# Optimization experiments

Hardware: AMD Instinct MI355X
Metric: run time of the kernel (lower is better)

The kernel has to match this reference:

```python
import jax, jax.numpy as jnp
import numpy as np


def _three_nn(parent_xyz, xyz):
    # parent_xyz: (bs, n, 3) queries; xyz: (bs, m, 3) reference points.
    # Squared pairwise distances (bs, n, m) without forming (x-y)^2 tensor of rank 4.
    d2 = (jnp.sum(parent_xyz**2, -1, keepdims=True)
          - 2.0 * jnp.einsum('bnd,bmd->bnm', parent_xyz, xyz)
          + jnp.sum(xyz**2, -1)[:, None, :])
    neg_d2, idx = jax.lax.top_k(-d2, 3)           # 3 smallest distances
    dist = jnp.sqrt(jnp.maximum(-neg_d2, 0.0))    # pointnet2 returns sqrt(dist2)
    return dist, idx                              # (bs, n, 3), (bs, n, 3)


def _three_interpolate(feats, idx, weight):
    # feats: (bs, c, m); idx, weight: (bs, n, 3) -> (bs, c, n)
    feats_t = jnp.swapaxes(feats, 1, 2)                     # (bs, m, c)
    gathered = jax.vmap(lambda f, i: f[i])(feats_t, idx)    # (bs, n, 3, c)
    out = jnp.einsum('bnkc,bnk->bcn', gathered, weight)
    return out


def _conv1x1(x, W, b):
    # x: (bs, c_in, n); W: (c_out, c_in); b: (c_out,)
    return jnp.einsum('oc,bcn->bon', W, x) + b[None, :, None]


def setup_inputs() -> dict:
    key = jax.random.key(0)
    ks = jax.random.split(key, 6)
    bs, m, n = 8, 1024, 4096
    c0, c1, c2 = 256, 128, 256
    xyz = jax.random.normal(ks[0], (bs, m, 3), jnp.float32)
    parent_xyz = jax.random.normal(ks[1], (bs, n, 3), jnp.float32)
    feats = jax.random.normal(ks[2], (bs, c0, m), jnp.float32)
    skip_feats = jax.random.normal(ks[3], (bs, c1, n), jnp.float32)
    W1 = jax.random.normal(ks[4], (c2, c0 + c1), jnp.float32) * (1.0 / np.sqrt(c0 + c1))
    b1 = jnp.zeros((c2,), jnp.float32)
    W2 = jax.random.normal(ks[5], (c2, c2), jnp.float32) * (1.0 / np.sqrt(c2))
    b2 = jnp.zeros((c2,), jnp.float32)
    return {"xyz": xyz, "parent_xyz": parent_xyz, "feats": feats,
            "skip_feats": skip_feats, "W1": W1, "b1": b1, "W2": W2, "b2": b2}


def reference(xyz, parent_xyz, feats, skip_feats, W1, b1, W2, b2):
    dist, idx = _three_nn(parent_xyz, xyz)
    inv_dist = 1.0 / (dist + 1e-8)
    weight = inv_dist / jnp.sum(inv_dist, 2, keepdims=True)     # (bs, n, 3)
    up_feats = _three_interpolate(feats, idx, weight)           # (bs, c0, n)
    parent_feats = jnp.concatenate([up_feats, skip_feats], 1)   # (bs, c0+c1, n)
    h = jax.nn.relu(_conv1x1(parent_feats, W1, b1))
    out = jax.nn.relu(_conv1x1(h, W2, b2))
    return out
```

## Files before the change

kernel.cpp:

```cpp
#include <hip/hip_runtime.h>
#include <hip/hip_bf16.h>
#include <cstddef>
#include <cstdint>

#define BS    8
#define M_PTS 1024
#define N_PTS 4096
#define C0    256
#define C1    128
#define C2    256
#define K1DIM 384

typedef __attribute__((ext_vector_type(8))) short bf16x8;
typedef __attribute__((ext_vector_type(4))) float f32x4;
typedef __attribute__((ext_vector_type(2))) float f32x2;

__device__ __forceinline__ ushort f2bf(float f) {
  union { float f; unsigned u; } v; v.f = f;
  unsigned r = v.u + 0x7fffu + ((v.u >> 16) & 1u);
  return (ushort)(r >> 16);
}

__device__ __forceinline__ float rdlane_f(float v, int lane) {
  union { float f; int i; } u; u.f = v;
  u.i = __builtin_amdgcn_readlane(u.i, lane);
  return u.f;
}

__device__ __forceinline__ f32x2 pk_mul(f32x2 a, f32x2 b) {
  f32x2 r; asm("v_pk_mul_f32 %0, %1, %2" : "=v"(r) : "v"(a), "v"(b)); return r;
}
__device__ __forceinline__ f32x2 pk_add(f32x2 a, f32x2 b) {
  f32x2 r; asm("v_pk_add_f32 %0, %1, %2" : "=v"(r) : "v"(a), "v"(b)); return r;
}

__global__ __launch_bounds__(256) void prep_k(
    const float* __restrict__ feats, const float* __restrict__ W1,
    const float* __restrict__ W2, float* __restrict__ featsT,
    ushort* __restrict__ W1f, ushort* __restrict__ W2f) {
  __shared__ float tile[32][33];
  const int t = threadIdx.x;
  if (blockIdx.x < 2048) {
    const int bx = blockIdx.x & 31;
    const int by = (blockIdx.x >> 5) & 7;
    const int bz = blockIdx.x >> 8;
    const int tx = t & 31, ty = t >> 5;
    const float* ip = feats + (size_t)bz * C0 * M_PTS;
    float*       op = featsT + (size_t)bz * C0 * M_PTS;
    const int r0 = by * 32, c0 = bx * 32;
#pragma unroll
    for (int i = 0; i < 4; ++i)
      tile[ty + i * 8][tx] = ip[(size_t)(r0 + ty + i * 8) * M_PTS + c0 + tx];
    __syncthreads();
#pragma unroll
    for (int i = 0; i < 4; ++i)
      op[(size_t)(c0 + ty + i * 8) * C0 + r0 + tx] = tile[tx][ty + i * 8];
  } else {
    const int id = (blockIdx.x - 2048) * 256 + t;
    if (id < C2 * K1DIM) {
      int m = id / K1DIM, k = id - m * K1DIM;
      int off = (((m >> 4) * 12 + (k >> 5)) * 4 + ((k >> 3) & 3)) * 128 + (m & 15) * 8 + (k & 7);
      W1f[off] = f2bf(W1[id]);
    }
    if (id < C2 * C2) {
      int m = id >> 8, k = id & 255;
      int off = (((m >> 4) * 8 + (k >> 5)) * 4 + ((k >> 3) & 3)) * 128 + (m & 15) * 8 + (k & 7);
      W2f[off] = f2bf(W2[id]);
    }
  }
}

__global__ __launch_bounds__(256, 4) void fp_fused_k(
    const float* __restrict__ xyz,
    const float* __restrict__ pxyz,
    const float* __restrict__ featsT,
    const float* __restrict__ skip,
    const ushort* __restrict__ W1f,
    const float* __restrict__ b1,
    const ushort* __restrict__ W2f,
    const float* __restrict__ b2,
    float* __restrict__ out) {
  __shared__ float4 smemq[2560];
  float4* pts4 = smemq;
  ushort* pfB  = (ushort*)(smemq + 1024);
  ushort* hbuf = (ushort*)smemq;

  const int t  = threadIdx.x;
  const int b  = blockIdx.x & 7;
  const int n0 = (blockIdx.x >> 3) * 32;
  const int wv = t >> 6, l = t & 63;
  const int q  = t >> 3, sub = t & 7;

  const float qx = pxyz[((size_t)b * N_PTS + n0 + q) * 3 + 0];
  const float qy = pxyz[((size_t)b * N_PTS + n0 + q) * 3 + 1];
  const float qz = pxyz[((size_t)b * N_PTS + n0 + q) * 3 + 2];

#pragma unroll
  for (int it = 0; it < 2; ++it) {
    const int p = t + it * 256;
    const float2* xb = (const float2*)(xyz + (size_t)b * 3 * M_PTS + 6 * p);
    const float2 A = xb[0], B = xb[1], C = xb[2];
    const float x0 = A.x, y0 = A.y, z0 = B.x, x1 = B.y, y1 = C.x, z1 = C.y;
    const float s0 = __fadd_rn(__fadd_rn(__fmul_rn(x0, x0), __fmul_rn(y0, y0)),
                               __fmul_rn(z0, z0));
    const float s1 = __fadd_rn(__fadd_rn(__fmul_rn(x1, x1), __fmul_rn(y1, y1)),
                               __fmul_rn(z1, z1));
    const int U = p ^ ((p >> 6) & 7);
    pts4[U * 2 + 0] = (float4){x0, x1, y0, y1};
    pts4[U * 2 + 1] = (float4){z0, z1, s0, s1};
  }

  float skp[16];
#pragma unroll
  for (int it = 0; it < 8; ++it) {
    const int id = t + it * 256;
    const int r2 = id >> 5, nn = id & 31;
    skp[2 * it + 0] = skip[((size_t)b * C1 + 2 * r2 + 0) * N_PTS + n0 + nn];
    skp[2 * it + 1] = skip[((size_t)b * C1 + 2 * r2 + 1) * N_PTS + n0 + nn];
  }

  const float qq = __fadd_rn(__fadd_rn(__fmul_rn(qx, qx), __fmul_rn(qy, qy)),
                             __fmul_rn(qz, qz));
  __syncthreads();

  float d0 = 3.4e38f, d1 = 3.4e38f, d2 = 3.4e38f;
  int   i0 = 0, i1 = 0, i2 = 0;
  {
    const f32x2 Qx2 = {qx, qx}, Qy2 = {qy, qy}, Qz2 = {qz, qz};
    const f32x2 Qq2 = {qq, qq}, Mn2 = {-2.0f, -2.0f};
    int pe[8];
#pragma unroll
    for (int e = 0; e < 8; ++e) pe[e] = (sub * 64 + (e ^ sub)) * 2;
    for (int jb = 0; jb < 8; ++jb) {
#pragma unroll
      for (int e = 0; e < 8; ++e) {
        const float4 lo = pts4[pe[e] + jb * 16];
        const float4 hi = pts4[pe[e] + jb * 16 + 1];
        const f32x2 Xp = {lo.x, lo.y}, Yp = {lo.z, lo.w};
        const f32x2 Zp = {hi.x, hi.y}, Sp = {hi.z, hi.w};
        const f32x2 dotp = pk_add(pk_add(pk_mul(Qx2, Xp), pk_mul(Qy2, Yp)),
                                  pk_mul(Qz2, Zp));
        const f32x2 dp = pk_add(pk_add(Qq2, pk_mul(dotp, Mn2)), Sp);
        {
          const float d = dp.x; const int m = jb * 16 + 2 * e;
          const bool c0 = d < d0, c1 = d < d1, c2 = d < d2;
          i2 = c1 ? i1 : (c2 ? m : i2);
          i1 = c0 ? i0 : (c1 ? m : i1);
          i0 = c0 ? m : i0;
          d2 = __builtin_amdgcn_fmed3f(d, d1, d2);
          d1 = __builtin_amdgcn_fmed3f(d, d0, d1);
          d0 = fminf(d, d0);
        }
        {
          const float d = dp.y; const int m = jb * 16 + 2 * e + 1;
          const bool c0 = d < d0, c1 = d < d1, c2 = d < d2;
          i2 = c1 ? i1 : (c2 ? m : i2);
          i1 = c0 ? i0 : (c1 ? m : i1);
          i0 = c0 ? m : i0;
          d2 = __builtin_amdgcn_fmed3f(d, d1, d2);
          d1 = __builtin_amdgcn_fmed3f(d, d0, d1);
          d0 = fminf(d, d0);
        }
      }
    }
    i0 += sub * 128; i1 += sub * 128; i2 += sub * 128;
  }

#pragma unroll
  for (int mk = 1; mk <= 4; mk <<= 1) {
    const float pd0 = __shfl_xor(d0, mk), pd1 = __shfl_xor(d1, mk), pd2 = __shfl_xor(d2, mk);
    const int   pi0 = __shfl_xor(i0, mk), pi1 = __shfl_xor(i1, mk), pi2 = __shfl_xor(i2, mk);
    const bool lo = (sub & mk) == 0;
    const float a0 = lo ? d0 : pd0, a1 = lo ? d1 : pd1, a2 = lo ? d2 : pd2;
    const float b0 = lo ? pd0 : d0, b1v = lo ? pd1 : d1, b2v = lo ? pd2 : d2;
    const int   A0 = lo ? i0 : pi0, A1 = lo ? i1 : pi1, A2 = lo ? i2 : pi2;
    const int   B0 = lo ? pi0 : i0, B1 = lo ? pi1 : i1, B2 = lo ? pi2 : i2;
    const bool c0 = b0 < a0;
    const bool cb1a0 = b1v < a0, cb0a1 = b0 < a1;
    const bool cb1a1 = b1v < a1, cb2a0 = b2v < a0, cb0a2 = b0 < a2;
    const float m0 = c0 ? b0 : a0;                 const int M0 = c0 ? B0 : A0;
    const float t1a = cb1a0 ? b1v : a0;            const int T1a = cb1a0 ? B1 : A0;
    const float t1b = cb0a1 ? b0 : a1;             const int T1b = cb0a1 ? B0 : A1;
    const float m1 = c0 ? t1a : t1b;               const int M1 = c0 ? T1a : T1b;
    const float sA = cb2a0 ? b2v : a0;             const int SA = cb2a0 ? B2 : A0;
    const float sB = cb1a1 ? b1v : a1;             const int SB = cb1a1 ? B1 : A1;
    const float sD = cb0a2 ? b0 : a2;              const int SD = cb0a2 ? B0 : A2;
    const float m2 = c0 ? (cb1a0 ? sA : sB) : (cb0a1 ? sB : sD);
    const int   M2 = c0 ? (cb1a0 ? SA : SB) : (cb0a1 ? SB : SD);
    d0 = m0; d1 = m1; d2 = m2; i0 = M0; i1 = M1; i2 = M2;
  }

  float w0f, w1f, w2f;
  {
    const float t0 = sqrtf(fmaxf(d0, 0.f)), t1 = sqrtf(fmaxf(d1, 0.f)),
                t2 = sqrtf(fmaxf(d2, 0.f));
    const float r0 = 1.0f / (t0 + 1e-8f), r1 = 1.0f / (t1 + 1e-8f),
                r2 = 1.0f / (t2 + 1e-8f);
    const float rs = __fadd_rn(__fadd_rn(r0, r1), r2);
    w0f = r0 / rs; w1f = r1 / rs; w2f = r2 / rs;
  }

  {
    const float* fb = featsT + (size_t)b * M_PTS * C0;
#pragma unroll
    for (int qi = 0; qi < 8; ++qi) {
      const int src = qi * 8;
      const int  j0 = __builtin_amdgcn_readlane(i0, src);
      const int  j1 = __builtin_amdgcn_readlane(i1, src);
      const int  j2 = __builtin_amdgcn_readlane(i2, src);
      const float w0 = rdlane_f(w0f, src), w1 = rdlane_f(w1f, src), w2 = rdlane_f(w2f, src);
      const float4 f0 = *(const float4*)(fb + (size_t)j0 * C0 + l * 4);
      const float4 f1 = *(const float4*)(fb + (size_t)j1 * C0 + l * 4);
      const float4 f2 = *(const float4*)(fb + (size_t)j2 * C0 + l * 4);
      ushort4 hv;
      hv.x = f2bf(w0 * f0.x + w1 * f1.x + w2 * f2.x);
      hv.y = f2bf(w0 * f0.y + w1 * f1.y + w2 * f2.y);
      hv.z = f2bf(w0 * f0.z + w1 * f1.z + w2 * f2.z);
      hv.w = f2bf(w0 * f0.w + w1 * f1.w + w2 * f2.w);
      const int nq = wv * 8 + qi;
      const int kq = l >> 1;
      const int u = kq * 32 + (nq ^ (kq & 7));
      *reinterpret_cast<ushort4*>(&pfB[u * 8 + (l & 1) * 4]) = hv;
    }
  }
#pragma unroll
  for (int it = 0; it < 8; ++it) {
    const int id = t + it * 256;
    const int r2 = id >> 5, nn = id & 31;
    const int k = C0 + 2 * r2;
    const int kq = k >> 3;
    const int u = kq * 32 + (nn ^ (kq & 7));
    ushort2 sv; sv.x = f2bf(skp[2 * it]); sv.y = f2bf(skp[2 * it + 1]);
    *reinterpret_cast<ushort2*>(&pfB[u * 8 + (k & 7)]) = sv;
  }
  __syncthreads();

  const int c = l & 15, g = l >> 4;

  f32x4 acc[4][2];
#pragma unroll
  for (int i = 0; i < 4; ++i)
#pragma unroll
    for (int j = 0; j < 2; ++j) acc[i][j] = (f32x4){0.f, 0.f, 0.f, 0.f};

  for (int kb = 0; kb < 12; ++kb) {
    const int kqg = kb * 4 + g;
    bf16x8 bfr[2], afr[4];
#pragma unroll
    for (int j = 0; j < 2; ++j)
      bfr[j] = *reinterpret_cast<const bf16x8*>(&pfB[(kqg * 32 + ((j * 16 + c) ^ (kqg & 7))) * 8]);
#pragma unroll
    for (int i = 0; i < 4; ++i)
      afr[i] = *reinterpret_cast<const bf16x8*>(&W1f[(((wv * 4 + i) * 12 + kb) * 4 + g) * 128 + c * 8]);
    __builtin_amdgcn_s_setprio(1);
#pragma unroll
    for (int i = 0; i < 4; ++i)
#pragma unroll
      for (int j = 0; j < 2; ++j)
        acc[i][j] = __builtin_amdgcn_mfma_f32_16x16x32_bf16(afr[i], bfr[j], acc[i][j], 0, 0, 0);
    __builtin_amdgcn_s_setprio(0);
  }

#pragma unroll
  for (int i = 0; i < 4; ++i) {
    const int mbase = wv * 64 + i * 16 + g * 4;
    const float4 bias = *(const float4*)(b1 + mbase);
#pragma unroll
    for (int j = 0; j < 2; ++j) {
      const int nn = j * 16 + c;
      const int kq = mbase >> 3;
      const int u = kq * 32 + (nn ^ (kq & 7));
      ushort4 hv;
      hv.x = f2bf(fmaxf(acc[i][j].x + bias.x, 0.f));
      hv.y = f2bf(fmaxf(acc[i][j].y + bias.y, 0.f));
      hv.z = f2bf(fmaxf(acc[i][j].z + bias.z, 0.f));
      hv.w = f2bf(fmaxf(acc[i][j].w + bias.w, 0.f));
      *reinterpret_cast<ushort4*>(&hbuf[u * 8 + (mbase & 7)]) = hv;
    }
  }
  __syncthreads();

#pragma unroll
  for (int i = 0; i < 4; ++i)
#pragma unroll
    for (int j = 0; j < 2; ++j) acc[i][j] = (f32x4){0.f, 0.f, 0.f, 0.f};

  for (int kb = 0; kb < 8; ++kb) {
    const int kqg = kb * 4 + g;
    bf16x8 bfr[2], afr[4];
#pragma unroll
    for (int j = 0; j < 2; ++j)
      bfr[j] = *reinterpret_cast<const bf16x8*>(&hbuf[(kqg * 32 + ((j * 16 + c) ^ (kqg & 7))) * 8]);
#pragma unroll
    for (int i = 0; i < 4; ++i)
      afr[i] = *reinterpret_cast<const bf16x8*>(&W2f[(((wv * 4 + i) * 8 + kb) * 4 + g) * 128 + c * 8]);
    __builtin_amdgcn_s_setprio(1);
#pragma unroll
    for (int i = 0; i < 4; ++i)
#pragma unroll
      for (int j = 0; j < 2; ++j)
        acc[i][j] = __builtin_amdgcn_mfma_f32_16x16x32_bf16(afr[i], bfr[j], acc[i][j], 0, 0, 0);
    __builtin_amdgcn_s_setprio(0);
  }

#pragma unroll
  for (int i = 0; i < 4; ++i) {
    const int mbase = wv * 64 + i * 16 + g * 4;
    const float4 bias = *(const float4*)(b2 + mbase);
#pragma unroll
    for (int j = 0; j < 2; ++j) {
      const int nn = n0 + j * 16 + c;
      out[((size_t)b * C2 + mbase + 0) * N_PTS + nn] = fmaxf(acc[i][j].x + bias.x, 0.f);
      out[((size_t)b * C2 + mbase + 1) * N_PTS + nn] = fmaxf(acc[i][j].y + bias.y, 0.f);
      out[((size_t)b * C2 + mbase + 2) * N_PTS + nn] = fmaxf(acc[i][j].z + bias.z, 0.f);
      out[((size_t)b * C2 + mbase + 3) * N_PTS + nn] = fmaxf(acc[i][j].w + bias.w, 0.f);
    }
  }
}

extern "C" void kernel_launch(void* const* d_in, const int* in_sizes, int n_in,
                              void* d_out, int out_size, void* d_ws, size_t ws_size,
                              hipStream_t stream) {
  const float* xyz   = (const float*)d_in[0];
  const float* pxyz  = (const float*)d_in[1];
  const float* feats = (const float*)d_in[2];
  const float* skip  = (const float*)d_in[3];
  const float* W1    = (const float*)d_in[4];
  const float* b1    = (const float*)d_in[5];
  const float* W2    = (const float*)d_in[6];
  const float* b2    = (const float*)d_in[7];
  float* out = (float*)d_out;

  float*  ws     = (float*)d_ws;
  float*  featsT = ws;
  ushort* W1f    = (ushort*)(featsT + (size_t)BS * M_PTS * C0);
  ushort* W2f    = W1f + (size_t)C2 * K1DIM;

  prep_k<<<2432, 256, 0, stream>>>(feats, W1, W2, featsT, W1f, W2f);
  fp_fused_k<<<BS * (N_PTS / 32), 256, 0, stream>>>(xyz, pxyz, featsT, skip,
                                                    W1f, b1, W2f, b2, out);
}
```

Measured before the change: 47.06 us.

## Split fused kernel into separate three-NN scan and GEMM kernels

Splits the single fused kernel into a nearest-neighbor scan kernel (16 queries per block, 16 lanes per query, occupancy hint of 8) and a GEMM kernel that reads indices and weights from a workspace buffer. The aim is to cut the register and LDS pressure of the fused kernel so each phase can run at higher occupancy. In exchange it adds a kernel launch and a round trip of indices and weights through global memory. It also adds a barrier before the hbuf writes, and skip loads are no longer held in registers across the scan.

```diff
diff --git a/kernel.cpp b/kernel.cpp
--- a/kernel.cpp
+++ b/kernel.cpp
@@ -19,12 +19,6 @@
   union { float f; unsigned u; } v; v.f = f;
   unsigned r = v.u + 0x7fffu + ((v.u >> 16) & 1u);
   return (ushort)(r >> 16);
-}
-
-__device__ __forceinline__ float rdlane_f(float v, int lane) {
-  union { float f; int i; } u; u.f = v;
-  u.i = __builtin_amdgcn_readlane(u.i, lane);
-  return u.f;
 }
 
 __device__ __forceinline__ f32x2 pk_mul(f32x2 a, f32x2 b) {
@@ -70,30 +64,14 @@
   }
 }
 
-__global__ __launch_bounds__(256, 4) void fp_fused_k(
-    const float* __restrict__ xyz,
-    const float* __restrict__ pxyz,
-    const float* __restrict__ featsT,
-    const float* __restrict__ skip,
-    const ushort* __restrict__ W1f,
-    const float* __restrict__ b1,
-    const ushort* __restrict__ W2f,
-    const float* __restrict__ b2,
-    float* __restrict__ out) {
-  __shared__ float4 smemq[2560];
-  float4* pts4 = smemq;
-  ushort* pfB  = (ushort*)(smemq + 1024);
-  ushort* hbuf = (ushort*)smemq;
-
+__global__ __launch_bounds__(256, 8) void nn_scan_k(
+    const float* __restrict__ xyz, const float* __restrict__ pxyz,
+    int* __restrict__ idx3, float* __restrict__ w3) {
+  __shared__ float4 pts4[1024];
   const int t  = threadIdx.x;
   const int b  = blockIdx.x & 7;
-  const int n0 = (blockIdx.x >> 3) * 32;
-  const int wv = t >> 6, l = t & 63;
-  const int q  = t >> 3, sub = t & 7;
-
-  const float qx = pxyz[((size_t)b * N_PTS + n0 + q) * 3 + 0];
-  const float qy = pxyz[((size_t)b * N_PTS + n0 + q) * 3 + 1];
-  const float qz = pxyz[((size_t)b * N_PTS + n0 + q) * 3 + 2];
+  const int n0 = (blockIdx.x >> 3) * 16;
+  const int q  = t >> 4, sub = t & 15;
 
 #pragma unroll
   for (int it = 0; it < 2; ++it) {
@@ -110,15 +88,10 @@
     pts4[U * 2 + 1] = (float4){z0, z1, s0, s1};
   }
 
-  float skp[16];
-#pragma unroll
-  for (int it = 0; it < 8; ++it) {
-    const int id = t + it * 256;
-    const int r2 = id >> 5, nn = id & 31;
-    skp[2 * it + 0] = skip[((size_t)b * C1 + 2 * r2 + 0) * N_PTS + n0 + nn];
-    skp[2 * it + 1] = skip[((size_t)b * C1 + 2 * r2 + 1) * N_PTS + n0 + nn];
-  }
-
+  const int gn = n0 + q;
+  const float qx = pxyz[((size_t)b * N_PTS + gn) * 3 + 0];
+  const float qy = pxyz[((size_t)b * N_PTS + gn) * 3 + 1];
+  const float qz = pxyz[((size_t)b * N_PTS + gn) * 3 + 2];
   const float qq = __fadd_rn(__fadd_rn(__fmul_rn(qx, qx), __fmul_rn(qy, qy)),
                              __fmul_rn(qz, qz));
   __syncthreads();
@@ -128,10 +101,11 @@
   {
     const f32x2 Qx2 = {qx, qx}, Qy2 = {qy, qy}, Qz2 = {qz, qz};
     const f32x2 Qq2 = {qq, qq}, Mn2 = {-2.0f, -2.0f};
+    const int stag = sub >> 1;
     int pe[8];
 #pragma unroll
-    for (int e = 0; e < 8; ++e) pe[e] = (sub * 64 + (e ^ sub)) * 2;
-    for (int jb = 0; jb < 8; ++jb) {
+    for (int e = 0; e < 8; ++e) pe[e] = (sub * 32 + (e ^ stag)) * 2;
+    for (int jb = 0; jb < 4; ++jb) {
 #pragma unroll
       for (int e = 0; e < 8; ++e) {
         const float4 lo = pts4[pe[e] + jb * 16];
@@ -163,11 +137,11 @@
         }
       }
     }
-    i0 += sub * 128; i1 += sub * 128; i2 += sub * 128;
-  }
-
-#pragma unroll
-  for (int mk = 1; mk <= 4; mk <<= 1) {
+    i0 += sub * 64; i1 += sub * 64; i2 += sub * 64;
+  }
+
+#pragma unroll
+  for (int mk = 1; mk <= 8; mk <<= 1) {
     const float pd0 = __shfl_xor(d0, mk), pd1 = __shfl_xor(d1, mk), pd2 = __shfl_xor(d2, mk);
     const int   pi0 = __shfl_xor(i0, mk), pi1 = __shfl_xor(i1, mk), pi2 = __shfl_xor(i2, mk);
     const bool lo = (sub & mk) == 0;
@@ -190,25 +164,52 @@
     d0 = m0; d1 = m1; d2 = m2; i0 = M0; i1 = M1; i2 = M2;
   }
 
-  float w0f, w1f, w2f;
-  {
+  if (sub == 0) {
     const float t0 = sqrtf(fmaxf(d0, 0.f)), t1 = sqrtf(fmaxf(d1, 0.f)),
                 t2 = sqrtf(fmaxf(d2, 0.f));
     const float r0 = 1.0f / (t0 + 1e-8f), r1 = 1.0f / (t1 + 1e-8f),
                 r2 = 1.0f / (t2 + 1e-8f);
     const float rs = __fadd_rn(__fadd_rn(r0, r1), r2);
-    w0f = r0 / rs; w1f = r1 / rs; w2f = r2 / rs;
-  }
+    const size_t base = ((size_t)b * N_PTS + gn) * 3;
+    idx3[base + 0] = i0; idx3[base + 1] = i1; idx3[base + 2] = i2;
+    w3[base + 0] = r0 / rs; w3[base + 1] = r1 / rs; w3[base + 2] = r2 / rs;
+  }
+}
+
+__global__ __launch_bounds__(256, 4) void gemm_k(
+    const float* __restrict__ featsT,
+    const float* __restrict__ skip,
+    const ushort* __restrict__ W1f,
+    const float* __restrict__ b1,
+    const ushort* __restrict__ W2f,
+    const float* __restrict__ b2,
+    const int* __restrict__ idx3, const float* __restrict__ w3,
+    float* __restrict__ out) {
+  __shared__ ushort pfB[12288];
+  __shared__ int   idx_s[32][3];
+  __shared__ float w_s[32][3];
+  ushort* hbuf = pfB;
+
+  const int t  = threadIdx.x;
+  const int b  = blockIdx.x & 7;
+  const int n0 = (blockIdx.x >> 3) * 32;
+  const int wv = t >> 6, l = t & 63;
+
+  if (t < 96) {
+    const int j = t / 3, k = t - 3 * j;
+    const size_t gg = ((size_t)b * N_PTS + n0 + j) * 3 + k;
+    idx_s[j][k] = idx3[gg];
+    w_s[j][k]   = w3[gg];
+  }
+  __syncthreads();
 
   {
     const float* fb = featsT + (size_t)b * M_PTS * C0;
 #pragma unroll
     for (int qi = 0; qi < 8; ++qi) {
-      const int src = qi * 8;
-      const int  j0 = __builtin_amdgcn_readlane(i0, src);
-      const int  j1 = __builtin_amdgcn_readlane(i1, src);
-      const int  j2 = __builtin_amdgcn_readlane(i2, src);
-      const float w0 = rdlane_f(w0f, src), w1 = rdlane_f(w1f, src), w2 = rdlane_f(w2f, src);
+      const int nq = wv * 8 + qi;
+      const int  j0 = idx_s[nq][0], j1 = idx_s[nq][1], j2 = idx_s[nq][2];
+      const float w0 = w_s[nq][0], w1 = w_s[nq][1], w2 = w_s[nq][2];
       const float4 f0 = *(const float4*)(fb + (size_t)j0 * C0 + l * 4);
       const float4 f1 = *(const float4*)(fb + (size_t)j1 * C0 + l * 4);
       const float4 f2 = *(const float4*)(fb + (size_t)j2 * C0 + l * 4);
@@ -217,7 +218,6 @@
       hv.y = f2bf(w0 * f0.y + w1 * f1.y + w2 * f2.y);
       hv.z = f2bf(w0 * f0.z + w1 * f1.z + w2 * f2.z);
       hv.w = f2bf(w0 * f0.w + w1 * f1.w + w2 * f2.w);
-      const int nq = wv * 8 + qi;
       const int kq = l >> 1;
       const int u = kq * 32 + (nq ^ (kq & 7));
       *reinterpret_cast<ushort4*>(&pfB[u * 8 + (l & 1) * 4]) = hv;
@@ -227,10 +227,12 @@
   for (int it = 0; it < 8; ++it) {
     const int id = t + it * 256;
     const int r2 = id >> 5, nn = id & 31;
+    const float s0v = skip[((size_t)b * C1 + 2 * r2 + 0) * N_PTS + n0 + nn];
+    const float s1v = skip[((size_t)b * C1 + 2 * r2 + 1) * N_PTS + n0 + nn];
     const int k = C0 + 2 * r2;
     const int kq = k >> 3;
     const int u = kq * 32 + (nn ^ (kq & 7));
-    ushort2 sv; sv.x = f2bf(skp[2 * it]); sv.y = f2bf(skp[2 * it + 1]);
+    ushort2 sv; sv.x = f2bf(s0v); sv.y = f2bf(s1v);
     *reinterpret_cast<ushort2*>(&pfB[u * 8 + (k & 7)]) = sv;
   }
   __syncthreads();
@@ -260,6 +262,7 @@
         acc[i][j] = __builtin_amdgcn_mfma_f32_16x16x32_bf16(afr[i], bfr[j], acc[i][j], 0, 0, 0);
     __builtin_amdgcn_s_setprio(0);
   }
+  __syncthreads();
 
 #pragma unroll
   for (int i = 0; i < 4; ++i) {
@@ -335,8 +338,11 @@
   float*  featsT = ws;
   ushort* W1f    = (ushort*)(featsT + (size_t)BS * M_PTS * C0);
   ushort* W2f    = W1f + (size_t)C2 * K1DIM;
-
+  int*    idx3   = (int*)(W2f + (size_t)C2 * C2);
+  float*  w3     = (float*)(idx3 + (size_t)BS * N_PTS * 3);
+
+  nn_scan_k<<<BS * (N_PTS / 16), 256, 0, stream>>>(xyz, pxyz, idx3, w3);
   prep_k<<<2432, 256, 0, stream>>>(feats, W1, W2, featsT, W1f, W2f);
-  fp_fused_k<<<BS * (N_PTS / 32), 256, 0, stream>>>(xyz, pxyz, featsT, skip,
-                                                    W1f, b1, W2f, b2, out);
-}
+  gemm_k<<<BS * (N_PTS / 32), 256, 0, stream>>>(featsT, skip, W1f, b1, W2f, b2,
+                                                idx3, w3, out);
+}
```

Result: slower. 58.35 us (+24.0%).

## Process two queries per thread in 3-NN search with 16-way split

Applied to the files above, without the earlier changes.

Each thread now handles two query points against 64 reference points instead of one query against 128, with 16 lanes cooperating per query pair. Each shared-memory load of a reference-point pair is reused for two distance computations, halving LDS traffic per distance. The shared-memory layout is split into separate lo/hi arrays with a new swizzle. The cost is one more shuffle-merge stage per query, two merges instead of one, and higher register pressure under the 4-wave occupancy bound.

```diff
diff --git a/kernel.cpp b/kernel.cpp
--- a/kernel.cpp
+++ b/kernel.cpp
@@ -34,140 +34,10 @@
   f32x2 r; asm("v_pk_add_f32 %0, %1, %2" : "=v"(r) : "v"(a), "v"(b)); return r;
 }
 
-__global__ __launch_bounds__(256) void prep_k(
-    const float* __restrict__ feats, const float* __restrict__ W1,
-    const float* __restrict__ W2, float* __restrict__ featsT,
-    ushort* __restrict__ W1f, ushort* __restrict__ W2f) {
-  __shared__ float tile[32][33];
-  const int t = threadIdx.x;
-  if (blockIdx.x < 2048) {
-    const int bx = blockIdx.x & 31;
-    const int by = (blockIdx.x >> 5) & 7;
-    const int bz = blockIdx.x >> 8;
-    const int tx = t & 31, ty = t >> 5;
-    const float* ip = feats + (size_t)bz * C0 * M_PTS;
-    float*       op = featsT + (size_t)bz * C0 * M_PTS;
-    const int r0 = by * 32, c0 = bx * 32;
-#pragma unroll
-    for (int i = 0; i < 4; ++i)
-      tile[ty + i * 8][tx] = ip[(size_t)(r0 + ty + i * 8) * M_PTS + c0 + tx];
-    __syncthreads();
-#pragma unroll
-    for (int i = 0; i < 4; ++i)
-      op[(size_t)(c0 + ty + i * 8) * C0 + r0 + tx] = tile[tx][ty + i * 8];
-  } else {
-    const int id = (blockIdx.x - 2048) * 256 + t;
-    if (id < C2 * K1DIM) {
-      int m = id / K1DIM, k = id - m * K1DIM;
-      int off = (((m >> 4) * 12 + (k >> 5)) * 4 + ((k >> 3) & 3)) * 128 + (m & 15) * 8 + (k & 7);
-      W1f[off] = f2bf(W1[id]);
-    }
-    if (id < C2 * C2) {
-      int m = id >> 8, k = id & 255;
-      int off = (((m >> 4) * 8 + (k >> 5)) * 4 + ((k >> 3) & 3)) * 128 + (m & 15) * 8 + (k & 7);
-      W2f[off] = f2bf(W2[id]);
-    }
-  }
-}
-
-__global__ __launch_bounds__(256, 4) void fp_fused_k(
-    const float* __restrict__ xyz,
-    const float* __restrict__ pxyz,
-    const float* __restrict__ featsT,
-    const float* __restrict__ skip,
-    const ushort* __restrict__ W1f,
-    const float* __restrict__ b1,
-    const ushort* __restrict__ W2f,
-    const float* __restrict__ b2,
-    float* __restrict__ out) {
-  __shared__ float4 smemq[2560];
-  float4* pts4 = smemq;
-  ushort* pfB  = (ushort*)(smemq + 1024);
-  ushort* hbuf = (ushort*)smemq;
-
-  const int t  = threadIdx.x;
-  const int b  = blockIdx.x & 7;
-  const int n0 = (blockIdx.x >> 3) * 32;
-  const int wv = t >> 6, l = t & 63;
-  const int q  = t >> 3, sub = t & 7;
-
-  const float qx = pxyz[((size_t)b * N_PTS + n0 + q) * 3 + 0];
-  const float qy = pxyz[((size_t)b * N_PTS + n0 + q) * 3 + 1];
-  const float qz = pxyz[((size_t)b * N_PTS + n0 + q) * 3 + 2];
-
-#pragma unroll
-  for (int it = 0; it < 2; ++it) {
-    const int p = t + it * 256;
-    const float2* xb = (const float2*)(xyz + (size_t)b * 3 * M_PTS + 6 * p);
-    const float2 A = xb[0], B = xb[1], C = xb[2];
-    const float x0 = A.x, y0 = A.y, z0 = B.x, x1 = B.y, y1 = C.x, z1 = C.y;
-    const float s0 = __fadd_rn(__fadd_rn(__fmul_rn(x0, x0), __fmul_rn(y0, y0)),
-                               __fmul_rn(z0, z0));
-    const float s1 = __fadd_rn(__fadd_rn(__fmul_rn(x1, x1), __fmul_rn(y1, y1)),
-                               __fmul_rn(z1, z1));
-    const int U = p ^ ((p >> 6) & 7);
-    pts4[U * 2 + 0] = (float4){x0, x1, y0, y1};
-    pts4[U * 2 + 1] = (float4){z0, z1, s0, s1};
-  }
-
-  float skp[16];
-#pragma unroll
-  for (int it = 0; it < 8; ++it) {
-    const int id = t + it * 256;
-    const int r2 = id >> 5, nn = id & 31;
-    skp[2 * it + 0] = skip[((size_t)b * C1 + 2 * r2 + 0) * N_PTS + n0 + nn];
-    skp[2 * it + 1] = skip[((size_t)b * C1 + 2 * r2 + 1) * N_PTS + n0 + nn];
-  }
-
-  const float qq = __fadd_rn(__fadd_rn(__fmul_rn(qx, qx), __fmul_rn(qy, qy)),
-                             __fmul_rn(qz, qz));
-  __syncthreads();
-
-  float d0 = 3.4e38f, d1 = 3.4e38f, d2 = 3.4e38f;
-  int   i0 = 0, i1 = 0, i2 = 0;
-  {
-    const f32x2 Qx2 = {qx, qx}, Qy2 = {qy, qy}, Qz2 = {qz, qz};
-    const f32x2 Qq2 = {qq, qq}, Mn2 = {-2.0f, -2.0f};
-    int pe[8];
-#pragma unroll
-    for (int e = 0; e < 8; ++e) pe[e] = (sub * 64 + (e ^ sub)) * 2;
-    for (int jb = 0; jb < 8; ++jb) {
-#pragma unroll
-      for (int e = 0; e < 8; ++e) {
-        const float4 lo = pts4[pe[e] + jb * 16];
-        const float4 hi = pts4[pe[e] + jb * 16 + 1];
-        const f32x2 Xp = {lo.x, lo.y}, Yp = {lo.z, lo.w};
-        const f32x2 Zp = {hi.x, hi.y}, Sp = {hi.z, hi.w};
-        const f32x2 dotp = pk_add(pk_add(pk_mul(Qx2, Xp), pk_mul(Qy2, Yp)),
-                                  pk_mul(Qz2, Zp));
-        const f32x2 dp = pk_add(pk_add(Qq2, pk_mul(dotp, Mn2)), Sp);
-        {
-          const float d = dp.x; const int m = jb * 16 + 2 * e;
-          const bool c0 = d < d0, c1 = d < d1, c2 = d < d2;
-          i2 = c1 ? i1 : (c2 ? m : i2);
-          i1 = c0 ? i0 : (c1 ? m : i1);
-          i0 = c0 ? m : i0;
-          d2 = __builtin_amdgcn_fmed3f(d, d1, d2);
-          d1 = __builtin_amdgcn_fmed3f(d, d0, d1);
-          d0 = fminf(d, d0);
-        }
-        {
-          const float d = dp.y; const int m = jb * 16 + 2 * e + 1;
-          const bool c0 = d < d0, c1 = d < d1, c2 = d < d2;
-          i2 = c1 ? i1 : (c2 ? m : i2);
-          i1 = c0 ? i0 : (c1 ? m : i1);
-          i0 = c0 ? m : i0;
-          d2 = __builtin_amdgcn_fmed3f(d, d1, d2);
-          d1 = __builtin_amdgcn_fmed3f(d, d0, d1);
-          d0 = fminf(d, d0);
-        }
-      }
-    }
-    i0 += sub * 128; i1 += sub * 128; i2 += sub * 128;
-  }
-
-#pragma unroll
-  for (int mk = 1; mk <= 4; mk <<= 1) {
+__device__ __forceinline__ void merge16(float& d0, float& d1, float& d2,
+                                        int& i0, int& i1, int& i2, int sub) {
+#pragma unroll
+  for (int mk = 1; mk <= 8; mk <<= 1) {
     const float pd0 = __shfl_xor(d0, mk), pd1 = __shfl_xor(d1, mk), pd2 = __shfl_xor(d2, mk);
     const int   pi0 = __shfl_xor(i0, mk), pi1 = __shfl_xor(i1, mk), pi2 = __shfl_xor(i2, mk);
     const bool lo = (sub & mk) == 0;
@@ -189,26 +59,216 @@
     const int   M2 = c0 ? (cb1a0 ? SA : SB) : (cb0a1 ? SB : SD);
     d0 = m0; d1 = m1; d2 = m2; i0 = M0; i1 = M1; i2 = M2;
   }
-
-  float w0f, w1f, w2f;
+}
+
+__global__ __launch_bounds__(256) void prep_k(
+    const float* __restrict__ feats, const float* __restrict__ W1,
+    const float* __restrict__ W2, float* __restrict__ featsT,
+    ushort* __restrict__ W1f, ushort* __restrict__ W2f) {
+  __shared__ float tile[32][33];
+  const int t = threadIdx.x;
+  if (blockIdx.x < 2048) {
+    const int bx = blockIdx.x & 31;
+    const int by = (blockIdx.x >> 5) & 7;
+    const int bz = blockIdx.x >> 8;
+    const int tx = t & 31, ty = t >> 5;
+    const float* ip = feats + (size_t)bz * C0 * M_PTS;
+    float*       op = featsT + (size_t)bz * C0 * M_PTS;
+    const int r0 = by * 32, c0 = bx * 32;
+#pragma unroll
+    for (int i = 0; i < 4; ++i)
+      tile[ty + i * 8][tx] = ip[(size_t)(r0 + ty + i * 8) * M_PTS + c0 + tx];
+    __syncthreads();
+#pragma unroll
+    for (int i = 0; i < 4; ++i)
+      op[(size_t)(c0 + ty + i * 8) * C0 + r0 + tx] = tile[tx][ty + i * 8];
+  } else {
+    const int id = (blockIdx.x - 2048) * 256 + t;
+    if (id < C2 * K1DIM) {
+      int m = id / K1DIM, k = id - m * K1DIM;
+      int off = (((m >> 4) * 12 + (k >> 5)) * 4 + ((k >> 3) & 3)) * 128 + (m & 15) * 8 + (k & 7);
+      W1f[off] = f2bf(W1[id]);
+    }
+    if (id < C2 * C2) {
+      int m = id >> 8, k = id & 255;
+      int off = (((m >> 4) * 8 + (k >> 5)) * 4 + ((k >> 3) & 3)) * 128 + (m & 15) * 8 + (k & 7);
+      W2f[off] = f2bf(W2[id]);
+    }
+  }
+}
+
+__global__ __launch_bounds__(256, 4) void fp_fused_k(
+    const float* __restrict__ xyz,
+    const float* __restrict__ pxyz,
+    const float* __restrict__ featsT,
+    const float* __restrict__ skip,
+    const ushort* __restrict__ W1f,
+    const float* __restrict__ b1,
+    const ushort* __restrict__ W2f,
+    const float* __restrict__ b2,
+    float* __restrict__ out) {
+  __shared__ float4 smemq[2560];
+  float4* loAr = smemq;
+  float4* hiAr = smemq + 512;
+  ushort* pfB  = (ushort*)(smemq + 1024);
+  ushort* hbuf = (ushort*)smemq;
+
+  const int t  = threadIdx.x;
+  const int b  = blockIdx.x & 7;
+  const int n0 = (blockIdx.x >> 3) * 32;
+  const int wv = t >> 6, l = t & 63;
+  const int qp = t >> 4, sub = t & 15;
+
+  const float qxa = pxyz[((size_t)b * N_PTS + n0 + qp) * 3 + 0];
+  const float qya = pxyz[((size_t)b * N_PTS + n0 + qp) * 3 + 1];
+  const float qza = pxyz[((size_t)b * N_PTS + n0 + qp) * 3 + 2];
+  const float qxb = pxyz[((size_t)b * N_PTS + n0 + qp + 16) * 3 + 0];
+  const float qyb = pxyz[((size_t)b * N_PTS + n0 + qp + 16) * 3 + 1];
+  const float qzb = pxyz[((size_t)b * N_PTS + n0 + qp + 16) * 3 + 2];
+
+#pragma unroll
+  for (int it = 0; it < 2; ++it) {
+    const int p = t + it * 256;
+    const float2* xb = (const float2*)(xyz + (size_t)b * 3 * M_PTS + 6 * p);
+    const float2 A = xb[0], B = xb[1], C = xb[2];
+    const float x0 = A.x, y0 = A.y, z0 = B.x, x1 = B.y, y1 = C.x, z1 = C.y;
+    const float s0 = __fadd_rn(__fadd_rn(__fmul_rn(x0, x0), __fmul_rn(y0, y0)),
+                               __fmul_rn(z0, z0));
+    const float s1 = __fadd_rn(__fadd_rn(__fmul_rn(x1, x1), __fmul_rn(y1, y1)),
+                               __fmul_rn(z1, z1));
+    const int U = p ^ ((p >> 5) & 7);
+    loAr[U] = (float4){x0, x1, y0, y1};
+    hiAr[U] = (float4){z0, z1, s0, s1};
+  }
+
+  float skp[16];
+#pragma unroll
+  for (int it = 0; it < 8; ++it) {
+    const int id = t + it * 256;
+    const int r2 = id >> 5, nn = id & 31;
+    skp[2 * it + 0] = skip[((size_t)b * C1 + 2 * r2 + 0) * N_PTS + n0 + nn];
+    skp[2 * it + 1] = skip[((size_t)b * C1 + 2 * r2 + 1) * N_PTS + n0 + nn];
+  }
+
+  const float qqa = __fadd_rn(__fadd_rn(__fmul_rn(qxa, qxa), __fmul_rn(qya, qya)),
+                              __fmul_rn(qza, qza));
+  const float qqb = __fadd_rn(__fadd_rn(__fmul_rn(qxb, qxb), __fmul_rn(qyb, qyb)),
+                              __fmul_rn(qzb, qzb));
+  __syncthreads();
+
+  float dA0 = 3.4e38f, dA1 = 3.4e38f, dA2 = 3.4e38f;
+  float dB0 = 3.4e38f, dB1 = 3.4e38f, dB2 = 3.4e38f;
+  int   iA0 = 0, iA1 = 0, iA2 = 0, iB0 = 0, iB1 = 0, iB2 = 0;
   {
-    const float t0 = sqrtf(fmaxf(d0, 0.f)), t1 = sqrtf(fmaxf(d1, 0.f)),
-                t2 = sqrtf(fmaxf(d2, 0.f));
+    const f32x2 QxA = {qxa, qxa}, QyA = {qya, qya}, QzA = {qza, qza}, QqA = {qqa, qqa};
+    const f32x2 QxB = {qxb, qxb}, QyB = {qyb, qyb}, QzB = {qzb, qzb}, QqB = {qqb, qqb};
+    const f32x2 Mn2 = {-2.0f, -2.0f};
+    const int base = sub * 32, sx = sub & 7;
+#pragma unroll
+    for (int jb = 0; jb < 4; ++jb) {
+#pragma unroll
+      for (int e = 0; e < 8; ++e) {
+        const int slot = base + jb * 8 + (e ^ sx);
+        const float4 lo = loAr[slot];
+        const float4 hi = hiAr[slot];
+        const f32x2 Xp = {lo.x, lo.y}, Yp = {lo.z, lo.w};
+        const f32x2 Zp = {hi.x, hi.y}, Sp = {hi.z, hi.w};
+        const int ml = jb * 16 + 2 * e;
+        {
+          const f32x2 dotp = pk_add(pk_add(pk_mul(QxA, Xp), pk_mul(QyA, Yp)),
+                                    pk_mul(QzA, Zp));
+          const f32x2 dp = pk_add(pk_add(QqA, pk_mul(dotp, Mn2)), Sp);
+          {
+            const float d = dp.x; const int m = ml;
+            const bool c0 = d < dA0, c1 = d < dA1, c2 = d < dA2;
+            iA2 = c1 ? iA1 : (c2 ? m : iA2);
+            iA1 = c0 ? iA0 : (c1 ? m : iA1);
+            iA0 = c0 ? m : iA0;
+            dA2 = __builtin_amdgcn_fmed3f(d, dA1, dA2);
+            dA1 = __builtin_amdgcn_fmed3f(d, dA0, dA1);
+            dA0 = fminf(d, dA0);
+          }
+          {
+            const float d = dp.y; const int m = ml + 1;
+            const bool c0 = d < dA0, c1 = d < dA1, c2 = d < dA2;
+            iA2 = c1 ? iA1 : (c2 ? m : iA2);
+            iA1 = c0 ? iA0 : (c1 ? m : iA1);
+            iA0 = c0 ? m : iA0;
+            dA2 = __builtin_amdgcn_fmed3f(d, dA1, dA2);
+            dA1 = __builtin_amdgcn_fmed3f(d, dA0, dA1);
+            dA0 = fminf(d, dA0);
+          }
+        }
+        {
+          const f32x2 dotp = pk_add(pk_add(pk_mul(QxB, Xp), pk_mul(QyB, Yp)),
+                                    pk_mul(QzB, Zp));
+          const f32x2 dp = pk_add(pk_add(QqB, pk_mul(dotp, Mn2)), Sp);
+          {
+            const float d = dp.x; const int m = ml;
+            const bool c0 = d < dB0, c1 = d < dB1, c2 = d < dB2;
+            iB2 = c1 ? iB1 : (c2 ? m : iB2);
+            iB1 = c0 ? iB0 : (c1 ? m : iB1);
+            iB0 = c0 ? m : iB0;
+            dB2 = __builtin_amdgcn_fmed3f(d, dB1, dB2);
+            dB1 = __builtin_amdgcn_fmed3f(d, dB0, dB1);
+            dB0 = fminf(d, dB0);
+          }
+          {
+            const float d = dp.y; const int m = ml + 1;
+            const bool c0 = d < dB0, c1 = d < dB1, c2 = d < dB2;
+            iB2 = c1 ? iB1 : (c2 ? m : iB2);
+            iB1 = c0 ? iB0 : (c1 ? m : iB1);
+            iB0 = c0 ? m : iB0;
+            dB2 = __builtin_amdgcn_fmed3f(d, dB1, dB2);
+            dB1 = __builtin_amdgcn_fmed3f(d, dB0, dB1);
+            dB0 = fminf(d, dB0);
+          }
+        }
+      }
+    }
+    iA0 += sub * 64; iA1 += sub * 64; iA2 += sub * 64;
+    iB0 += sub * 64; iB1 += sub * 64; iB2 += sub * 64;
+  }
+
+  merge16(dA0, dA1, dA2, iA0, iA1, iA2, sub);
+  merge16(dB0, dB1, dB2, iB0, iB1, iB2, sub);
+
+  float wA0, wA1, wA2, wB0, wB1, wB2;
+  {
+    const float t0 = sqrtf(fmaxf(dA0, 0.f)), t1 = sqrtf(fmaxf(dA1, 0.f)),
+                t2 = sqrtf(fmaxf(dA2, 0.f));
     const float r0 = 1.0f / (t0 + 1e-8f), r1 = 1.0f / (t1 + 1e-8f),
                 r2 = 1.0f / (t2 + 1e-8f);
     const float rs = __fadd_rn(__fadd_rn(r0, r1), r2);
-    w0f = r0 / rs; w1f = r1 / rs; w2f = r2 / rs;
+    wA0 = r0 / rs; wA1 = r1 / rs; wA2 = r2 / rs;
+  }
+  {
+    const float t0 = sqrtf(fmaxf(dB0, 0.f)), t1 = sqrtf(fmaxf(dB1, 0.f)),
+                t2 = sqrtf(fmaxf(dB2, 0.f));
+    const float r0 = 1.0f / (t0 + 1e-8f), r1 = 1.0f / (t1 + 1e-8f),
+                r2 = 1.0f / (t2 + 1e-8f);
+    const float rs = __fadd_rn(__fadd_rn(r0, r1), r2);
+    wB0 = r0 / rs; wB1 = r1 / rs; wB2 = r2 / rs;
   }
 
   {
     const float* fb = featsT + (size_t)b * M_PTS * C0;
 #pragma unroll
     for (int qi = 0; qi < 8; ++qi) {
-      const int src = qi * 8;
-      const int  j0 = __builtin_amdgcn_readlane(i0, src);
-      const int  j1 = __builtin_amdgcn_readlane(i1, src);
-      const int  j2 = __builtin_amdgcn_readlane(i2, src);
-      const float w0 = rdlane_f(w0f, src), w1 = rdlane_f(w1f, src), w2 = rdlane_f(w2f, src);
+      const int src = (qi & 3) * 16;
+      int j0, j1, j2; float w0, w1, w2;
+      if (qi < 4) {
+        j0 = __builtin_amdgcn_readlane(iA0, src);
+        j1 = __builtin_amdgcn_readlane(iA1, src);
+        j2 = __builtin_amdgcn_readlane(iA2, src);
+        w0 = rdlane_f(wA0, src); w1 = rdlane_f(wA1, src); w2 = rdlane_f(wA2, src);
+      } else {
+        j0 = __builtin_amdgcn_readlane(iB0, src);
+        j1 = __builtin_amdgcn_readlane(iB1, src);
+        j2 = __builtin_amdgcn_readlane(iB2, src);
+        w0 = rdlane_f(wB0, src); w1 = rdlane_f(wB1, src); w2 = rdlane_f(wB2, src);
+      }
+      const int nq = wv * 4 + (qi & 3) + ((qi >> 2) << 4);
       const float4 f0 = *(const float4*)(fb + (size_t)j0 * C0 + l * 4);
       const float4 f1 = *(const float4*)(fb + (size_t)j1 * C0 + l * 4);
       const float4 f2 = *(const float4*)(fb + (size_t)j2 * C0 + l * 4);
@@ -217,7 +277,6 @@
       hv.y = f2bf(w0 * f0.y + w1 * f1.y + w2 * f2.y);
       hv.z = f2bf(w0 * f0.z + w1 * f1.z + w2 * f2.z);
       hv.w = f2bf(w0 * f0.w + w1 * f1.w + w2 * f2.w);
-      const int nq = wv * 8 + qi;
       const int kq = l >> 1;
       const int u = kq * 32 + (nq ^ (kq & 7));
       *reinterpret_cast<ushort4*>(&pfB[u * 8 + (l & 1) * 4]) = hv;
```

Measured after the change: 48.42 us. +2.9%, slower.

## Halve queries per block, split points across 16 lanes, shrink LDS to raise occupancy

Applied to the files above, without the earlier changes.

Each block now handles 16 query points instead of 32. Each query's 3-NN scan is spread over 16 lanes with a 4-step shuffle merge, and the LDS footprint drops from 40KB to 16KB by aliasing the point buffer with the feature and hidden buffers behind extra barriers. Launch bounds are raised to 6 blocks per CU, packed-FP32 asm is replaced by scalar math with pre-doubled coordinates, and the bf16 conversion uses the intrinsic. In exchange, every block re-stages all 1024 reference points and the W1/W2 fragments for half as many queries, and each MFMA stage issues one column tile per weight fragment, so redundant loads and the number of blocks both double.

```diff
diff --git a/kernel.cpp b/kernel.cpp
--- a/kernel.cpp
+++ b/kernel.cpp
@@ -13,25 +13,19 @@
 
 typedef __attribute__((ext_vector_type(8))) short bf16x8;
 typedef __attribute__((ext_vector_type(4))) float f32x4;
-typedef __attribute__((ext_vector_type(2))) float f32x2;
 
 __device__ __forceinline__ ushort f2bf(float f) {
   union { float f; unsigned u; } v; v.f = f;
   unsigned r = v.u + 0x7fffu + ((v.u >> 16) & 1u);
   return (ushort)(r >> 16);
 }
-
+__device__ __forceinline__ ushort bf16c(float f) {
+  return __builtin_bit_cast(ushort, __float2bfloat16(f));
+}
 __device__ __forceinline__ float rdlane_f(float v, int lane) {
   union { float f; int i; } u; u.f = v;
   u.i = __builtin_amdgcn_readlane(u.i, lane);
   return u.f;
-}
-
-__device__ __forceinline__ f32x2 pk_mul(f32x2 a, f32x2 b) {
-  f32x2 r; asm("v_pk_mul_f32 %0, %1, %2" : "=v"(r) : "v"(a), "v"(b)); return r;
-}
-__device__ __forceinline__ f32x2 pk_add(f32x2 a, f32x2 b) {
-  f32x2 r; asm("v_pk_add_f32 %0, %1, %2" : "=v"(r) : "v"(a), "v"(b)); return r;
 }
 
 __global__ __launch_bounds__(256) void prep_k(
@@ -70,7 +64,7 @@
   }
 }
 
-__global__ __launch_bounds__(256, 4) void fp_fused_k(
+__global__ __launch_bounds__(256, 6) void fp_fused_k(
     const float* __restrict__ xyz,
     const float* __restrict__ pxyz,
     const float* __restrict__ featsT,
@@ -80,16 +74,17 @@
     const ushort* __restrict__ W2f,
     const float* __restrict__ b2,
     float* __restrict__ out) {
-  __shared__ float4 smemq[2560];
-  float4* pts4 = smemq;
-  ushort* pfB  = (ushort*)(smemq + 1024);
+  __shared__ float4 smemq[1024];
+  float4* loAr = smemq;
+  float4* hiAr = smemq + 512;
+  ushort* pfB  = (ushort*)smemq;
   ushort* hbuf = (ushort*)smemq;
 
   const int t  = threadIdx.x;
   const int b  = blockIdx.x & 7;
-  const int n0 = (blockIdx.x >> 3) * 32;
+  const int n0 = (blockIdx.x >> 3) * 16;
   const int wv = t >> 6, l = t & 63;
-  const int q  = t >> 3, sub = t & 7;
+  const int q  = t >> 4, sub = t & 15;
 
   const float qx = pxyz[((size_t)b * N_PTS + n0 + q) * 3 + 0];
   const float qy = pxyz[((size_t)b * N_PTS + n0 + q) * 3 + 1];
@@ -105,18 +100,16 @@
                                __fmul_rn(z0, z0));
     const float s1 = __fadd_rn(__fadd_rn(__fmul_rn(x1, x1), __fmul_rn(y1, y1)),
                                __fmul_rn(z1, z1));
-    const int U = p ^ ((p >> 6) & 7);
-    pts4[U * 2 + 0] = (float4){x0, x1, y0, y1};
-    pts4[U * 2 + 1] = (float4){z0, z1, s0, s1};
-  }
-
-  float skp[16];
+    const int U = p ^ ((p >> 5) & 7);
+    loAr[U] = (float4){x0 + x0, x1 + x1, y0 + y0, y1 + y1};
+    hiAr[U] = (float4){z0 + z0, z1 + z1, s0, s1};
+  }
+
+  float skp[8];
 #pragma unroll
   for (int it = 0; it < 8; ++it) {
-    const int id = t + it * 256;
-    const int r2 = id >> 5, nn = id & 31;
-    skp[2 * it + 0] = skip[((size_t)b * C1 + 2 * r2 + 0) * N_PTS + n0 + nn];
-    skp[2 * it + 1] = skip[((size_t)b * C1 + 2 * r2 + 1) * N_PTS + n0 + nn];
+    const int r2 = it * 16 + (t >> 4), nn = t & 15;
+    skp[it] = skip[((size_t)b * C1 + r2) * N_PTS + n0 + nn];
   }
 
   const float qq = __fadd_rn(__fadd_rn(__fmul_rn(qx, qx), __fmul_rn(qy, qy)),
@@ -126,23 +119,19 @@
   float d0 = 3.4e38f, d1 = 3.4e38f, d2 = 3.4e38f;
   int   i0 = 0, i1 = 0, i2 = 0;
   {
-    const f32x2 Qx2 = {qx, qx}, Qy2 = {qy, qy}, Qz2 = {qz, qz};
-    const f32x2 Qq2 = {qq, qq}, Mn2 = {-2.0f, -2.0f};
-    int pe[8];
-#pragma unroll
-    for (int e = 0; e < 8; ++e) pe[e] = (sub * 64 + (e ^ sub)) * 2;
-    for (int jb = 0; jb < 8; ++jb) {
+    const int su = sub & 7, base = sub * 32;
+#pragma unroll
+    for (int jb = 0; jb < 4; ++jb) {
 #pragma unroll
       for (int e = 0; e < 8; ++e) {
-        const float4 lo = pts4[pe[e] + jb * 16];
-        const float4 hi = pts4[pe[e] + jb * 16 + 1];
-        const f32x2 Xp = {lo.x, lo.y}, Yp = {lo.z, lo.w};
-        const f32x2 Zp = {hi.x, hi.y}, Sp = {hi.z, hi.w};
-        const f32x2 dotp = pk_add(pk_add(pk_mul(Qx2, Xp), pk_mul(Qy2, Yp)),
-                                  pk_mul(Qz2, Zp));
-        const f32x2 dp = pk_add(pk_add(Qq2, pk_mul(dotp, Mn2)), Sp);
+        const int slot = base + jb * 8 + (e ^ su);
+        const float4 A  = loAr[slot];
+        const float4 Bv = hiAr[slot];
         {
-          const float d = dp.x; const int m = jb * 16 + 2 * e;
+          const float dot2 = __fadd_rn(__fadd_rn(__fmul_rn(qx, A.x), __fmul_rn(qy, A.z)),
+                                       __fmul_rn(qz, Bv.x));
+          const float d = __fadd_rn(__fsub_rn(qq, dot2), Bv.z);
+          const int m = (jb * 8 + e) * 2;
           const bool c0 = d < d0, c1 = d < d1, c2 = d < d2;
           i2 = c1 ? i1 : (c2 ? m : i2);
           i1 = c0 ? i0 : (c1 ? m : i1);
@@ -152,7 +141,10 @@
           d0 = fminf(d, d0);
         }
         {
-          const float d = dp.y; const int m = jb * 16 + 2 * e + 1;
+          const float dot2 = __fadd_rn(__fadd_rn(__fmul_rn(qx, A.y), __fmul_rn(qy, A.w)),
+                                       __fmul_rn(qz, Bv.y));
+          const float d = __fadd_rn(__fsub_rn(qq, dot2), Bv.w);
+          const int m = (jb * 8 + e) * 2 + 1;
           const bool c0 = d < d0, c1 = d < d1, c2 = d < d2;
           i2 = c1 ? i1 : (c2 ? m : i2);
           i1 = c0 ? i0 : (c1 ? m : i1);
@@ -163,11 +155,11 @@
         }
       }
     }
-    i0 += sub * 128; i1 += sub * 128; i2 += sub * 128;
-  }
-
-#pragma unroll
-  for (int mk = 1; mk <= 4; mk <<= 1) {
+    i0 += sub * 64; i1 += sub * 64; i2 += sub * 64;
+  }
+
+#pragma unroll
+  for (int mk = 1; mk <= 8; mk <<= 1) {
     const float pd0 = __shfl_xor(d0, mk), pd1 = __shfl_xor(d1, mk), pd2 = __shfl_xor(d2, mk);
     const int   pi0 = __shfl_xor(i0, mk), pi1 = __shfl_xor(i1, mk), pi2 = __shfl_xor(i2, mk);
     const bool lo = (sub & mk) == 0;
@@ -199,12 +191,13 @@
     const float rs = __fadd_rn(__fadd_rn(r0, r1), r2);
     w0f = r0 / rs; w1f = r1 / rs; w2f = r2 / rs;
   }
+  __syncthreads();
 
   {
     const float* fb = featsT + (size_t)b * M_PTS * C0;
 #pragma unroll
-    for (int qi = 0; qi < 8; ++qi) {
-      const int src = qi * 8;
+    for (int qi = 0; qi < 4; ++qi) {
+      const int src = qi * 16;
       const int  j0 = __builtin_amdgcn_readlane(i0, src);
       const int  j1 = __builtin_amdgcn_readlane(i1, src);
       const int  j2 = __builtin_amdgcn_readlane(i2, src);
@@ -213,93 +206,77 @@
       const float4 f1 = *(const float4*)(fb + (size_t)j1 * C0 + l * 4);
       const float4 f2 = *(const float4*)(fb + (size_t)j2 * C0 + l * 4);
       ushort4 hv;
-      hv.x = f2bf(w0 * f0.x + w1 * f1.x + w2 * f2.x);
-      hv.y = f2bf(w0 * f0.y + w1 * f1.y + w2 * f2.y);
-      hv.z = f2bf(w0 * f0.z + w1 * f1.z + w2 * f2.z);
-      hv.w = f2bf(w0 * f0.w + w1 * f1.w + w2 * f2.w);
-      const int nq = wv * 8 + qi;
+      hv.x = bf16c(w0 * f0.x + w1 * f1.x + w2 * f2.x);
+      hv.y = bf16c(w0 * f0.y + w1 * f1.y + w2 * f2.y);
+      hv.z = bf16c(w0 * f0.z + w1 * f1.z + w2 * f2.z);
+      hv.w = bf16c(w0 * f0.w + w1 * f1.w + w2 * f2.w);
+      const int nq = wv * 4 + qi;
       const int kq = l >> 1;
-      const int u = kq * 32 + (nq ^ (kq & 7));
+      const int u = kq * 16 + (nq ^ (kq & 7));
       *reinterpret_cast<ushort4*>(&pfB[u * 8 + (l & 1) * 4]) = hv;
     }
   }
 #pragma unroll
   for (int it = 0; it < 8; ++it) {
-    const int id = t + it * 256;
-    const int r2 = id >> 5, nn = id & 31;
-    const int k = C0 + 2 * r2;
+    const int r2 = it * 16 + (t >> 4), nn = t & 15;
+    const int k = C0 + r2;
     const int kq = k >> 3;
-    const int u = kq * 32 + (nn ^ (kq & 7));
-    ushort2 sv; sv.x = f2bf(skp[2 * it]); sv.y = f2bf(skp[2 * it + 1]);
-    *reinterpret_cast<ushort2*>(&pfB[u * 8 + (k & 7)]) = sv;
+    pfB[(kq * 16 + (nn ^ (kq & 7))) * 8 + (k & 7)] = bf16c(skp[it]);
   }
   __syncthreads();
 
   const int c = l & 15, g = l >> 4;
 
-  f32x4 acc[4][2];
-#pragma unroll
-  for (int i = 0; i < 4; ++i)
-#pragma unroll
-    for (int j = 0; j < 2; ++j) acc[i][j] = (f32x4){0.f, 0.f, 0.f, 0.f};
+  f32x4 acc[4];
+#pragma unroll
+  for (int i = 0; i < 4; ++i) acc[i] = (f32x4){0.f, 0.f, 0.f, 0.f};
 
   for (int kb = 0; kb < 12; ++kb) {
     const int kqg = kb * 4 + g;
-    bf16x8 bfr[2], afr[4];
-#pragma unroll
-    for (int j = 0; j < 2; ++j)
-      bfr[j] = *reinterpret_cast<const bf16x8*>(&pfB[(kqg * 32 + ((j * 16 + c) ^ (kqg & 7))) * 8]);
+    const bf16x8 bfr = *reinterpret_cast<const bf16x8*>(
+        &pfB[(kqg * 16 + (c ^ (kqg & 7))) * 8]);
+    bf16x8 afr[4];
 #pragma unroll
     for (int i = 0; i < 4; ++i)
       afr[i] = *reinterpret_cast<const bf16x8*>(&W1f[(((wv * 4 + i) * 12 + kb) * 4 + g) * 128 + c * 8]);
     __builtin_amdgcn_s_setprio(1);
 #pragma unroll
     for (int i = 0; i < 4; ++i)
-#pragma unroll
-      for (int j = 0; j < 2; ++j)
-        acc[i][j] = __builtin_amdgcn_mfma_f32_16x16x32_bf16(afr[i], bfr[j], acc[i][j], 0, 0, 0);
+      acc[i] = __builtin_amdgcn_mfma_f32_16x16x32_bf16(afr[i], bfr, acc[i], 0, 0, 0);
     __builtin_amdgcn_s_setprio(0);
   }
+  __syncthreads();
 
 #pragma unroll
   for (int i = 0; i < 4; ++i) {
     const int mbase = wv * 64 + i * 16 + g * 4;
     const float4 bias = *(const float4*)(b1 + mbase);
-#pragma unroll
-    for (int j = 0; j < 2; ++j) {
-      const int nn = j * 16 + c;
-      const int kq = mbase >> 3;
-      const int u = kq * 32 + (nn ^ (kq & 7));
-      ushort4 hv;
-      hv.x = f2bf(fmaxf(acc[i][j].x + bias.x, 0.f));
-      hv.y = f2bf(fmaxf(acc[i][j].y + bias.y, 0.f));
-      hv.z = f2bf(fmaxf(acc[i][j].z + bias.z, 0.f));
-      hv.w = f2bf(fmaxf(acc[i][j].w + bias.w, 0.f));
-      *reinterpret_cast<ushort4*>(&hbuf[u * 8 + (mbase & 7)]) = hv;
-    }
-  }
-  __syncthreads();
-
-#pragma unroll
-  for (int i = 0; i < 4; ++i)
-#pragma unroll
-    for (int j = 0; j < 2; ++j) acc[i][j] = (f32x4){0.f, 0.f, 0.f, 0.f};
+    const int kq = mbase >> 3;
+    const int u = kq * 16 + (c ^ (kq & 7));
+    ushort4 hv;
+    hv.x = bf16c(fmaxf(acc[i].x + bias.x, 0.f));
+    hv.y = bf16c(fmaxf(acc[i].y + bias.y, 0.f));
+    hv.z = bf16c(fmaxf(acc[i].z + bias.z, 0.f));
+    hv.w = bf16c(fmaxf(acc[i].w + bias.w, 0.f));
+    *reinterpret_cast<ushort4*>(&hbuf[u * 8 + (mbase & 7)]) = hv;
+  }
+  __syncthreads();
+
+#pragma unroll
+  for (int i = 0; i < 4; ++i) acc[i] = (f32x4){0.f, 0.f, 0.f, 0.f};
 
   for (int kb = 0; kb < 8; ++kb) {
     const int kqg = kb * 4 + g;
-    bf16x8 bfr[2], afr[4];
-#pragma unroll
-    for (int j = 0; j < 2; ++j)
-      bfr[j] = *reinterpret_cast<const bf16x8*>(&hbuf[(kqg * 32 + ((j * 16 + c) ^ (kqg & 7))) * 8]);
+    const bf16x8 bfr = *reinterpret_cast<const bf16x8*>(
+        &hbuf[(kqg * 16 + (c ^ (kqg & 7))) * 8]);
+    bf16x8 afr[4];
 #pragma unroll
     for (int i = 0; i < 4; ++i)
       afr[i] = *reinterpret_cast<const bf16x8*>(&W2f[(((wv * 4 + i) * 8 + kb) * 4 + g) * 128 + c * 8]);
     __builtin_amdgcn_s_setprio(1);
 #pragma unroll
     for (int i = 0; i < 4; ++i)
-#pragma unroll
-      for (int j = 0; j < 2; ++j)
-        acc[i][j] = __builtin_amdgcn_mfma_f32_16x16x32_bf16(afr[i], bfr[j], acc[i][j], 0, 0, 0);
+      acc[i] = __builtin_amdgcn_mfma_f32_16x16x32_bf16(afr[i], bfr, acc[i], 0, 0, 0);
     __builtin_amdgcn_s_setprio(0);
   }
 
@@ -307,14 +284,11 @@
   for (int i = 0; i < 4; ++i) {
     const int mbase = wv * 64 + i * 16 + g * 4;
     const float4 bias = *(const float4*)(b2 + mbase);
-#pragma unroll
-    for (int j = 0; j < 2; ++j) {
-      const int nn = n0 + j * 16 + c;
-      out[((size_t)b * C2 + mbase + 0) * N_PTS + nn] = fmaxf(acc[i][j].x + bias.x, 0.f);
-      out[((size_t)b * C2 + mbase + 1) * N_PTS + nn] = fmaxf(acc[i][j].y + bias.y, 0.f);
-      out[((size_t)b * C2 + mbase + 2) * N_PTS + nn] = fmaxf(acc[i][j].z + bias.z, 0.f);
-      out[((size_t)b * C2 + mbase + 3) * N_PTS + nn] = fmaxf(acc[i][j].w + bias.w, 0.f);
-    }
+    const int nn = n0 + c;
+    out[((size_t)b * C2 + mbase + 0) * N_PTS + nn] = fmaxf(acc[i].x + bias.x, 0.f);
+    out[((size_t)b * C2 + mbase + 1) * N_PTS + nn] = fmaxf(acc[i].y + bias.y, 0.f);
+    out[((size_t)b * C2 + mbase + 2) * N_PTS + nn] = fmaxf(acc[i].z + bias.z, 0.f);
+    out[((size_t)b * C2 + mbase + 3) * N_PTS + nn] = fmaxf(acc[i].w + bias.w, 0.f);
   }
 }
 
@@ -337,6 +311,6 @@
   ushort* W2f    = W1f + (size_t)C2 * K1DIM;
 
   prep_k<<<2432, 256, 0, stream>>>(feats, W1, W2, featsT, W1f, W2f);
-  fp_fused_k<<<BS * (N_PTS / 32), 256, 0, stream>>>(xyz, pxyz, featsT, skip,
+  fp_fused_k<<<BS * (N_PTS / 16), 256, 0, stream>>>(xyz, pxyz, featsT, skip,
                                                     W1f, b1, W2f, b2, out);
 }
```

New measurement: 52.79 us. 1.12x slower.
